# Kernel optimization log

Measured on AMD Instinct MI355X. Metric: run time of the kernel, lower is better.

The kernel has to match this reference:

```python
import jax, jax.numpy as jnp
import numpy as np

K = 7          # kernel_size
GC = 16        # group_channels (hardcoded in module)
EPS = 1e-5     # BatchNorm eps


def setup_inputs() -> dict:
    key = jax.random.key(0)
    ks = jax.random.split(key, 4)
    B, C, H, W = 4, 256, 56, 56
    Cr = C // 4                      # reduction_ratio = 4
    G = C // GC                      # groups = 16
    return {
        "x": jax.random.normal(ks[0], (B, C, H, W), jnp.float32),
        "conv1_w": jax.random.normal(ks[1], (Cr, C), jnp.float32) * 0.05,
        "bn_gamma": jnp.ones((Cr,), jnp.float32),
        "bn_beta": jnp.zeros((Cr,), jnp.float32),
        "bn_mean": jnp.zeros((Cr,), jnp.float32),
        "bn_var": jnp.ones((Cr,), jnp.float32),
        "conv2_w": jax.random.normal(ks[2], (K * K * G, Cr), jnp.float32) * 0.05,
        "conv2_b": jax.random.normal(ks[3], (K * K * G,), jnp.float32) * 0.05,
    }


def _unfold(x, k):
    # torch nn.Unfold with padding=(k-1)//2, stride=1 -> [B, C, k*k, H, W]
    B, C, H, W = x.shape
    p = (k - 1) // 2
    xp = jnp.pad(x, ((0, 0), (0, 0), (p, p), (p, p)))
    patches = jnp.stack(
        [xp[:, :, i:i + H, j:j + W] for i in range(k) for j in range(k)],
        axis=2,
    )  # (kh, kw) flattened, channel-slowest -> matches torch unfold layout
    return patches


def reference(x, conv1_w, bn_gamma, bn_beta, bn_mean, bn_var, conv2_w, conv2_b):
    B, C, H, W = x.shape
    G = C // GC
    # kernel-generation branch (stride == 1, no avgpool)
    w = jnp.einsum('bchw,oc->bohw', x, conv1_w)                 # conv1 1x1
    inv_std = jax.lax.rsqrt(bn_var + EPS)
    w = (w - bn_mean[None, :, None, None]) * (bn_gamma * inv_std)[None, :, None, None] \
        + bn_beta[None, :, None, None]                           # BN (eval)
    w = jax.nn.relu(w)
    w = jnp.einsum('bchw,oc->bohw', w, conv2_w) + conv2_b[None, :, None, None]
    w = w.reshape(B, G, K * K, H, W)                             # [B,G,K2,H,W]
    # unfold + weighted reduce
    patches = _unfold(x, K).reshape(B, G, GC, K * K, H, W)       # [B,G,gc,K2,H,W]
    out = jnp.einsum('bgkhw,bgckhw->bgchw', w, patches)          # sum over K2
    return out.reshape(B, C, H, W)
```

## Files before the change

### kernel.cpp

```cpp
#include <hip/hip_runtime.h>


#define EPS 1e-5f

typedef __fp16 half2t __attribute__((ext_vector_type(2)));
typedef __fp16 half4t __attribute__((ext_vector_type(4)));
typedef __fp16 half8t __attribute__((ext_vector_type(8)));
typedef float floatx4 __attribute__((ext_vector_type(4)));

__global__ __launch_bounds__(256) void k0_setup(
    const float* __restrict__ w1, const float* __restrict__ gamma,
    const float* __restrict__ beta, const float* __restrict__ mean,
    const float* __restrict__ var, const float* __restrict__ cw,
    __fp16* __restrict__ w1fh, float* __restrict__ b1f,
    __fp16* __restrict__ cwb)
{
    const int tid = blockIdx.x * 256 + threadIdx.x;
    const int n   = gridDim.x * 256;
    for (int idx = tid; idx < 16384; idx += n) {
        int c2 = idx >> 7, r = idx & 127, o = r >> 1, c = 2 * c2 + (r & 1);
        float s = gamma[o] * rsqrtf(var[o] + EPS);
        w1fh[idx] = (__fp16)(w1[o * 256 + c] * s);
    }
    for (int idx = tid; idx < 64; idx += n) {
        float s = gamma[idx] * rsqrtf(var[idx] + EPS);
        b1f[idx] = beta[idx] - mean[idx] * s;
    }
    for (int idx = tid; idx < 65536; idx += n) {
        int g = idx >> 12, k = (idx >> 6) & 63, c = idx & 63;
        cwb[idx] = (__fp16)((k < 49) ? cw[(g * 49 + k) * 64 + c] : 0.f);
    }
}

__global__ __launch_bounds__(256, 4) void k1_conv1(
    const float* __restrict__ x, const __fp16* __restrict__ w1fh,
    const float* __restrict__ b1f, __fp16* __restrict__ mid)
{
    __shared__ __align__(16) __fp16 lx2[32 * 136];
    __shared__ __align__(16) __fp16 lwh[32 * 128];
    const int t   = threadIdx.x;
    const int b   = blockIdx.y;
    const int p0  = blockIdx.x * 64;
    const int o4  = (t >> 4) * 4;
    const int px4 = (t & 15) * 4;
    float acc[4][4] = {};

    for (int c0 = 0; c0 < 256; c0 += 64) {
        {
            int c2 = t >> 3, px8 = (t & 7) * 8;
            const float* r0 = &x[(size_t)(b * 256 + c0 + 2 * c2) * 3136 + p0 + px8];
            const float* r1 = r0 + 3136;
            float4 a0 = *(const float4*)r0, a1 = *(const float4*)(r0 + 4);
            float4 b0 = *(const float4*)r1, b1 = *(const float4*)(r1 + 4);
            half8t lo, hi;
            half2t q;
            q = __builtin_amdgcn_cvt_pkrtz(a0.x, b0.x); lo[0]=q[0]; lo[1]=q[1];
            q = __builtin_amdgcn_cvt_pkrtz(a0.y, b0.y); lo[2]=q[0]; lo[3]=q[1];
            q = __builtin_amdgcn_cvt_pkrtz(a0.z, b0.z); lo[4]=q[0]; lo[5]=q[1];
            q = __builtin_amdgcn_cvt_pkrtz(a0.w, b0.w); lo[6]=q[0]; lo[7]=q[1];
            q = __builtin_amdgcn_cvt_pkrtz(a1.x, b1.x); hi[0]=q[0]; hi[1]=q[1];
            q = __builtin_amdgcn_cvt_pkrtz(a1.y, b1.y); hi[2]=q[0]; hi[3]=q[1];
            q = __builtin_amdgcn_cvt_pkrtz(a1.z, b1.z); hi[4]=q[0]; hi[5]=q[1];
            q = __builtin_amdgcn_cvt_pkrtz(a1.w, b1.w); hi[6]=q[0]; hi[7]=q[1];
            *(half8t*)&lx2[c2 * 136 + px8 * 2]     = lo;
            *(half8t*)&lx2[c2 * 136 + px8 * 2 + 8] = hi;
        }
#pragma unroll
        for (int i = 0; i < 2; ++i) {
            int s = t + i * 256;
            *(half8t*)&lwh[s * 8] = *(const half8t*)&w1fh[c0 * 64 + s * 8];
        }
        __syncthreads();
#pragma unroll 4
        for (int c2 = 0; c2 < 32; ++c2) {
            half8t mv = *(const half8t*)&lx2[c2 * 136 + px4 * 2];
            half8t wv = *(const half8t*)&lwh[c2 * 128 + o4 * 2];
            half2t mp[4], wp[4];
#pragma unroll
            for (int j = 0; j < 4; ++j) {
                mp[j][0] = mv[2 * j]; mp[j][1] = mv[2 * j + 1];
                wp[j][0] = wv[2 * j]; wp[j][1] = wv[2 * j + 1];
            }
#pragma unroll
            for (int i = 0; i < 4; ++i)
#pragma unroll
                for (int j = 0; j < 4; ++j)
                    acc[i][j] = __builtin_amdgcn_fdot2(wp[i], mp[j], acc[i][j], false);
        }
        __syncthreads();
    }
    float bb[4];
#pragma unroll
    for (int i = 0; i < 4; ++i) bb[i] = b1f[o4 + i];
#pragma unroll
    for (int j = 0; j < 4; ++j) {
        int p = p0 + px4 + j;
        float v0 = fmaxf(acc[0][j] + bb[0], 0.f);
        float v1 = fmaxf(acc[1][j] + bb[1], 0.f);
        float v2 = fmaxf(acc[2][j] + bb[2], 0.f);
        float v3 = fmaxf(acc[3][j] + bb[3], 0.f);
        half2t u0 = __builtin_amdgcn_cvt_pkrtz(v0, v1);
        half2t u1 = __builtin_amdgcn_cvt_pkrtz(v2, v3);
        half4t h; h[0] = u0[0]; h[1] = u0[1]; h[2] = u1[0]; h[3] = u1[1];
        *(half4t*)&mid[(size_t)(b * 3136 + p) * 64 + o4] = h;
    }
}

__global__ __launch_bounds__(256, 5) void k23_fused(
    const float* __restrict__ x, const __fp16* __restrict__ mid,
    const __fp16* __restrict__ cwb, const float* __restrict__ cb,
    float* __restrict__ out)
{
    __shared__ __align__(16) unsigned char smem[31760];
    __fp16* lmid = (__fp16*)smem;
    __fp16* lwk  = (__fp16*)(smem + 9216);
    float*  lx   = (float*)smem;
    float*  lw2  = (float*)(smem + 18432);

    const int t  = threadIdx.x;
    const int b  = blockIdx.z;
    const int g  = blockIdx.y;
    const int th = blockIdx.x / 7, tw = blockIdx.x % 7;
    const int h0 = th * 8, w0 = tw * 8;

#pragma unroll
    for (int i = 0; i < 2; ++i) {
        int s  = t + i * 256;
        int px = s >> 3, c8 = s & 7;
        int pix = (h0 + (px >> 3)) * 56 + w0 + (px & 7);
        *(half8t*)&lmid[px * 72 + c8 * 8] =
            *(const half8t*)&mid[(size_t)(b * 3136 + pix) * 64 + c8 * 8];
    }
#pragma unroll
    for (int i = 0; i < 2; ++i) {
        int s = t + i * 256;
        int k = s >> 3, c8 = s & 7;
        *(half8t*)&lwk[k * 72 + c8 * 8] = *(const half8t*)&cwb[g * 4096 + s * 8];
    }
    float rv[13];
#pragma unroll
    for (int i = 0; i < 13; ++i) {
        int idx = t + i * 256;
        float v = 0.f;
        if (idx < 3136) {
            int ch = idx / 196, r = idx % 196;
            int rr = r / 14, col = r % 14;
            int gh = h0 + rr - 3, gw = w0 + col - 3;
            if (gh >= 0 && gh < 56 && gw >= 0 && gw < 56)
                v = x[(b * 256 + g * 16 + ch) * 3136 + gh * 56 + gw];
        }
        rv[i] = v;
    }
    __syncthreads();

    {
        const int lane = t & 63, wvid = t >> 6;
        const int mrow = lane & 15, quad = lane >> 4;
        half8t a0 = *(const half8t*)&lwk[(wvid * 16 + mrow) * 72 + quad * 8];
        half8t a1 = *(const half8t*)&lwk[(wvid * 16 + mrow) * 72 + quad * 8 + 32];
        float bias[4];
        int   kor[4];
#pragma unroll
        for (int i = 0; i < 4; ++i) {
            kor[i]  = wvid * 16 + quad * 4 + i;
            bias[i] = (kor[i] < 49) ? cb[g * 49 + kor[i]] : 0.f;
        }
#pragma unroll
        for (int pt = 0; pt < 4; ++pt) {
            half8t b0 = *(const half8t*)&lmid[(pt * 16 + mrow) * 72 + quad * 8];
            half8t b1 = *(const half8t*)&lmid[(pt * 16 + mrow) * 72 + quad * 8 + 32];
            floatx4 acc = {0.f, 0.f, 0.f, 0.f};
            acc = __builtin_amdgcn_mfma_f32_16x16x32_f16(a0, b0, acc, 0, 0, 0);
            acc = __builtin_amdgcn_mfma_f32_16x16x32_f16(a1, b1, acc, 0, 0, 0);
#pragma unroll
            for (int i = 0; i < 4; ++i)
                if (kor[i] < 49)
                    lw2[kor[i] * 68 + pt * 16 + mrow] = acc[i] + bias[i];
        }
    }
    __syncthreads();

#pragma unroll
    for (int i = 0; i < 13; ++i) {
        int idx = t + i * 256;
        if (idx < 3136) {
            int ch = idx / 196, r = idx % 196;
            lx[ch * 232 + (r / 14) * 15 + (r % 14)] = rv[i];
        }
    }
    __syncthreads();

    const int cc = t >> 4, pxt = t & 15;
    const int sh = pxt >> 1, sw4 = (pxt & 1) * 4;
    float a0 = 0.f, a1 = 0.f, a2 = 0.f, a3 = 0.f;
#pragma unroll
    for (int kh = 0; kh < 7; ++kh) {
        float xr[10];
        const int base = cc * 232 + (sh + kh) * 15 + sw4;
#pragma unroll
        for (int j = 0; j < 10; ++j) xr[j] = lx[base + j];
#pragma unroll
        for (int kw = 0; kw < 7; ++kw) {
            const float4 wv = *(const float4*)&lw2[(kh * 7 + kw) * 68 + pxt * 4];
            a0 = fmaf(wv.x, xr[kw + 0], a0);
            a1 = fmaf(wv.y, xr[kw + 1], a1);
            a2 = fmaf(wv.z, xr[kw + 2], a2);
            a3 = fmaf(wv.w, xr[kw + 3], a3);
        }
    }
    *(float4*)&out[(b * 256 + g * 16 + cc) * 3136 + (h0 + sh) * 56 + w0 + sw4] =
        make_float4(a0, a1, a2, a3);
}

extern "C" void kernel_launch(void* const* d_in, const int* in_sizes, int n_in,
                              void* d_out, int out_size, void* d_ws, size_t ws_size,
                              hipStream_t stream) {
    const float* x     = (const float*)d_in[0];
    const float* w1    = (const float*)d_in[1];
    const float* gamma = (const float*)d_in[2];
    const float* beta  = (const float*)d_in[3];
    const float* mean  = (const float*)d_in[4];
    const float* var   = (const float*)d_in[5];
    const float* cw    = (const float*)d_in[6];
    const float* cb    = (const float*)d_in[7];
    float* out = (float*)d_out;

    unsigned char* ws = (unsigned char*)d_ws;
    __fp16* mid  = (__fp16*)(ws);
    __fp16* w1fh = (__fp16*)(ws + 1605632);
    float*  b1f  = (float*)(ws + 1638400);
    __fp16* cwb  = (__fp16*)(ws + 1638656);

    k0_setup<<<dim3(64), 256, 0, stream>>>(w1, gamma, beta, mean, var, cw,
                                           w1fh, b1f, cwb);
    k1_conv1<<<dim3(49, 4), 256, 0, stream>>>(x, w1fh, b1f, mid);
    k23_fused<<<dim3(49, 16, 4), 256, 0, stream>>>(x, mid, cwb, cb, out);
}
```

Baseline: 113.5 us.

## Use MFMA for conv1, load conv2 weights directly, vectorize unfold LDS reads

Rewrites the 1x1 conv1 kernel to use 16x16x32 fp16 MFMA with weights held in registers instead of fdot2 on CUDA-style tiles. The output is staged through LDS for coalesced half8 stores, and the setup kernel's weight layout changes to row-major to match. In the fused kernel, conv2 A-fragments are loaded straight from global memory instead of through LDS, which shrinks shared memory. The x tile row pitch changes to 16 so that rows can be read as float4. The risks are lower occupancy in conv1 (launch bounds drop to 2) and reduced overlap of the global weight loads.

```diff
diff --git a/kernel.cpp b/kernel.cpp
--- a/kernel.cpp
+++ b/kernel.cpp
@@ -4,7 +4,6 @@
 #define EPS 1e-5f
 
 typedef __fp16 half2t __attribute__((ext_vector_type(2)));
-typedef __fp16 half4t __attribute__((ext_vector_type(4)));
 typedef __fp16 half8t __attribute__((ext_vector_type(8)));
 typedef float floatx4 __attribute__((ext_vector_type(4)));
 
@@ -18,9 +17,9 @@
     const int tid = blockIdx.x * 256 + threadIdx.x;
     const int n   = gridDim.x * 256;
     for (int idx = tid; idx < 16384; idx += n) {
-        int c2 = idx >> 7, r = idx & 127, o = r >> 1, c = 2 * c2 + (r & 1);
+        int o = idx >> 8;
         float s = gamma[o] * rsqrtf(var[o] + EPS);
-        w1fh[idx] = (__fp16)(w1[o * 256 + c] * s);
+        w1fh[idx] = (__fp16)(w1[idx] * s);
     }
     for (int idx = tid; idx < 64; idx += n) {
         float s = gamma[idx] * rsqrtf(var[idx] + EPS);
@@ -32,77 +31,73 @@
     }
 }
 
-__global__ __launch_bounds__(256, 4) void k1_conv1(
+__global__ __launch_bounds__(256, 2) void k1_conv1(
     const float* __restrict__ x, const __fp16* __restrict__ w1fh,
     const float* __restrict__ b1f, __fp16* __restrict__ mid)
 {
-    __shared__ __align__(16) __fp16 lx2[32 * 136];
-    __shared__ __align__(16) __fp16 lwh[32 * 128];
-    const int t   = threadIdx.x;
-    const int b   = blockIdx.y;
-    const int p0  = blockIdx.x * 64;
-    const int o4  = (t >> 4) * 4;
-    const int px4 = (t & 15) * 4;
-    float acc[4][4] = {};
-
-    for (int c0 = 0; c0 < 256; c0 += 64) {
-        {
-            int c2 = t >> 3, px8 = (t & 7) * 8;
-            const float* r0 = &x[(size_t)(b * 256 + c0 + 2 * c2) * 3136 + p0 + px8];
-            const float* r1 = r0 + 3136;
-            float4 a0 = *(const float4*)r0, a1 = *(const float4*)(r0 + 4);
-            float4 b0 = *(const float4*)r1, b1 = *(const float4*)(r1 + 4);
-            half8t lo, hi;
-            half2t q;
-            q = __builtin_amdgcn_cvt_pkrtz(a0.x, b0.x); lo[0]=q[0]; lo[1]=q[1];
-            q = __builtin_amdgcn_cvt_pkrtz(a0.y, b0.y); lo[2]=q[0]; lo[3]=q[1];
-            q = __builtin_amdgcn_cvt_pkrtz(a0.z, b0.z); lo[4]=q[0]; lo[5]=q[1];
-            q = __builtin_amdgcn_cvt_pkrtz(a0.w, b0.w); lo[6]=q[0]; lo[7]=q[1];
-            q = __builtin_amdgcn_cvt_pkrtz(a1.x, b1.x); hi[0]=q[0]; hi[1]=q[1];
-            q = __builtin_amdgcn_cvt_pkrtz(a1.y, b1.y); hi[2]=q[0]; hi[3]=q[1];
-            q = __builtin_amdgcn_cvt_pkrtz(a1.z, b1.z); hi[4]=q[0]; hi[5]=q[1];
-            q = __builtin_amdgcn_cvt_pkrtz(a1.w, b1.w); hi[6]=q[0]; hi[7]=q[1];
-            *(half8t*)&lx2[c2 * 136 + px8 * 2]     = lo;
-            *(half8t*)&lx2[c2 * 136 + px8 * 2 + 8] = hi;
-        }
-#pragma unroll
-        for (int i = 0; i < 2; ++i) {
-            int s = t + i * 256;
-            *(half8t*)&lwh[s * 8] = *(const half8t*)&w1fh[c0 * 64 + s * 8];
+    __shared__ __align__(16) __fp16 lxB[64 * 72];
+    const int t    = threadIdx.x;
+    const int b    = blockIdx.y;
+    const int p0   = blockIdx.x * 64;
+    const int lane = t & 63, wvid = t >> 6;
+    const int mrow = lane & 15, quad = lane >> 4;
+
+    const int orow = wvid * 16 + mrow;
+    half8t A[4][2];
+#pragma unroll
+    for (int ch = 0; ch < 4; ++ch)
+#pragma unroll
+        for (int h = 0; h < 2; ++h)
+            A[ch][h] = *(const half8t*)&w1fh[orow * 256 + ch * 64 + h * 32 + quad * 8];
+
+    floatx4 acc[4] = {};
+    const int c2 = t & 31, pxo = t >> 5;
+    for (int ch = 0; ch < 4; ++ch) {
+        const float* r0 = &x[(size_t)(b * 256 + ch * 64 + 2 * c2) * 3136 + p0 + pxo * 8];
+        const float* r1 = r0 + 3136;
+        float4 a0 = *(const float4*)r0, a1 = *(const float4*)(r0 + 4);
+        float4 b0 = *(const float4*)r1, b1 = *(const float4*)(r1 + 4);
+        const float* f0 = (const float*)&a0;
+        const float* f1 = (const float*)&b0;
+#pragma unroll
+        for (int j = 0; j < 4; ++j) {
+            half2t q = __builtin_amdgcn_cvt_pkrtz(f0[j], f1[j]);
+            *(half2t*)&lxB[(pxo * 8 + j) * 72 + 2 * c2] = q;
+        }
+        const float* g0 = (const float*)&a1;
+        const float* g1 = (const float*)&b1;
+#pragma unroll
+        for (int j = 0; j < 4; ++j) {
+            half2t q = __builtin_amdgcn_cvt_pkrtz(g0[j], g1[j]);
+            *(half2t*)&lxB[(pxo * 8 + 4 + j) * 72 + 2 * c2] = q;
         }
         __syncthreads();
-#pragma unroll 4
-        for (int c2 = 0; c2 < 32; ++c2) {
-            half8t mv = *(const half8t*)&lx2[c2 * 136 + px4 * 2];
-            half8t wv = *(const half8t*)&lwh[c2 * 128 + o4 * 2];
-            half2t mp[4], wp[4];
-#pragma unroll
-            for (int j = 0; j < 4; ++j) {
-                mp[j][0] = mv[2 * j]; mp[j][1] = mv[2 * j + 1];
-                wp[j][0] = wv[2 * j]; wp[j][1] = wv[2 * j + 1];
-            }
-#pragma unroll
-            for (int i = 0; i < 4; ++i)
-#pragma unroll
-                for (int j = 0; j < 4; ++j)
-                    acc[i][j] = __builtin_amdgcn_fdot2(wp[i], mp[j], acc[i][j], false);
+#pragma unroll
+        for (int pt = 0; pt < 4; ++pt) {
+            half8t bf0 = *(const half8t*)&lxB[(pt * 16 + mrow) * 72 + quad * 8];
+            half8t bf1 = *(const half8t*)&lxB[(pt * 16 + mrow) * 72 + quad * 8 + 32];
+            acc[pt] = __builtin_amdgcn_mfma_f32_16x16x32_f16(A[ch][0], bf0, acc[pt], 0, 0, 0);
+            acc[pt] = __builtin_amdgcn_mfma_f32_16x16x32_f16(A[ch][1], bf1, acc[pt], 0, 0, 0);
         }
         __syncthreads();
     }
     float bb[4];
 #pragma unroll
-    for (int i = 0; i < 4; ++i) bb[i] = b1f[o4 + i];
-#pragma unroll
-    for (int j = 0; j < 4; ++j) {
-        int p = p0 + px4 + j;
-        float v0 = fmaxf(acc[0][j] + bb[0], 0.f);
-        float v1 = fmaxf(acc[1][j] + bb[1], 0.f);
-        float v2 = fmaxf(acc[2][j] + bb[2], 0.f);
-        float v3 = fmaxf(acc[3][j] + bb[3], 0.f);
-        half2t u0 = __builtin_amdgcn_cvt_pkrtz(v0, v1);
-        half2t u1 = __builtin_amdgcn_cvt_pkrtz(v2, v3);
-        half4t h; h[0] = u0[0]; h[1] = u0[1]; h[2] = u1[0]; h[3] = u1[1];
-        *(half4t*)&mid[(size_t)(b * 3136 + p) * 64 + o4] = h;
+    for (int i = 0; i < 4; ++i) bb[i] = b1f[wvid * 16 + quad * 4 + i];
+#pragma unroll
+    for (int pt = 0; pt < 4; ++pt)
+#pragma unroll
+        for (int i = 0; i < 4; ++i) {
+            float v = fmaxf(acc[pt][i] + bb[i], 0.f);
+            lxB[(pt * 16 + mrow) * 72 + wvid * 16 + quad * 4 + i] = (__fp16)v;
+        }
+    __syncthreads();
+#pragma unroll
+    for (int it = 0; it < 2; ++it) {
+        int slot = t + it * 256;
+        int px = slot >> 3, o8 = slot & 7;
+        *(half8t*)&mid[(size_t)(b * 3136 + p0 + px) * 64 + o8 * 8] =
+            *(const half8t*)&lxB[px * 72 + o8 * 8];
     }
 }
 
@@ -111,17 +106,21 @@
     const __fp16* __restrict__ cwb, const float* __restrict__ cb,
     float* __restrict__ out)
 {
-    __shared__ __align__(16) unsigned char smem[31760];
+    __shared__ __align__(16) unsigned char smem[27920];
     __fp16* lmid = (__fp16*)smem;
-    __fp16* lwk  = (__fp16*)(smem + 9216);
     float*  lx   = (float*)smem;
-    float*  lw2  = (float*)(smem + 18432);
+    float*  lw2  = (float*)(smem + 14592);
 
     const int t  = threadIdx.x;
     const int b  = blockIdx.z;
     const int g  = blockIdx.y;
     const int th = blockIdx.x / 7, tw = blockIdx.x % 7;
     const int h0 = th * 8, w0 = tw * 8;
+    const int lane = t & 63, wvid = t >> 6;
+    const int mrow = lane & 15, quad = lane >> 4;
+
+    half8t a0 = *(const half8t*)&cwb[g * 4096 + (wvid * 16 + mrow) * 64 + quad * 8];
+    half8t a1 = *(const half8t*)&cwb[g * 4096 + (wvid * 16 + mrow) * 64 + quad * 8 + 32];
 
 #pragma unroll
     for (int i = 0; i < 2; ++i) {
@@ -130,12 +129,6 @@
         int pix = (h0 + (px >> 3)) * 56 + w0 + (px & 7);
         *(half8t*)&lmid[px * 72 + c8 * 8] =
             *(const half8t*)&mid[(size_t)(b * 3136 + pix) * 64 + c8 * 8];
-    }
-#pragma unroll
-    for (int i = 0; i < 2; ++i) {
-        int s = t + i * 256;
-        int k = s >> 3, c8 = s & 7;
-        *(half8t*)&lwk[k * 72 + c8 * 8] = *(const half8t*)&cwb[g * 4096 + s * 8];
     }
     float rv[13];
 #pragma unroll
@@ -154,10 +147,6 @@
     __syncthreads();
 
     {
-        const int lane = t & 63, wvid = t >> 6;
-        const int mrow = lane & 15, quad = lane >> 4;
-        half8t a0 = *(const half8t*)&lwk[(wvid * 16 + mrow) * 72 + quad * 8];
-        half8t a1 = *(const half8t*)&lwk[(wvid * 16 + mrow) * 72 + quad * 8 + 32];
         float bias[4];
         int   kor[4];
 #pragma unroll
@@ -185,31 +174,35 @@
         int idx = t + i * 256;
         if (idx < 3136) {
             int ch = idx / 196, r = idx % 196;
-            lx[ch * 232 + (r / 14) * 15 + (r % 14)] = rv[i];
+            lx[ch * 228 + (r / 14) * 16 + (r % 14)] = rv[i];
         }
     }
     __syncthreads();
 
     const int cc = t >> 4, pxt = t & 15;
     const int sh = pxt >> 1, sw4 = (pxt & 1) * 4;
-    float a0 = 0.f, a1 = 0.f, a2 = 0.f, a3 = 0.f;
+    float a0f = 0.f, a1f = 0.f, a2f = 0.f, a3f = 0.f;
 #pragma unroll
     for (int kh = 0; kh < 7; ++kh) {
-        float xr[10];
-        const int base = cc * 232 + (sh + kh) * 15 + sw4;
-#pragma unroll
-        for (int j = 0; j < 10; ++j) xr[j] = lx[base + j];
+        const float* row = &lx[cc * 228 + (sh + kh) * 16 + sw4];
+        float4 x0 = *(const float4*)row;
+        float4 x1 = *(const float4*)(row + 4);
+        float4 x2 = *(const float4*)(row + 8);
+        float xr[12];
+        xr[0] = x0.x; xr[1] = x0.y; xr[2]  = x0.z; xr[3]  = x0.w;
+        xr[4] = x1.x; xr[5] = x1.y; xr[6]  = x1.z; xr[7]  = x1.w;
+        xr[8] = x2.x; xr[9] = x2.y; xr[10] = x2.z; xr[11] = x2.w;
 #pragma unroll
         for (int kw = 0; kw < 7; ++kw) {
             const float4 wv = *(const float4*)&lw2[(kh * 7 + kw) * 68 + pxt * 4];
-            a0 = fmaf(wv.x, xr[kw + 0], a0);
-            a1 = fmaf(wv.y, xr[kw + 1], a1);
-            a2 = fmaf(wv.z, xr[kw + 2], a2);
-            a3 = fmaf(wv.w, xr[kw + 3], a3);
+            a0f = fmaf(wv.x, xr[kw + 0], a0f);
+            a1f = fmaf(wv.y, xr[kw + 1], a1f);
+            a2f = fmaf(wv.z, xr[kw + 2], a2f);
+            a3f = fmaf(wv.w, xr[kw + 3], a3f);
         }
     }
     *(float4*)&out[(b * 256 + g * 16 + cc) * 3136 + (h0 + sh) * 56 + w0 + sw4] =
-        make_float4(a0, a1, a2, a3);
+        make_float4(a0f, a1f, a2f, a3f);
 }
 
 extern "C" void kernel_launch(void* const* d_in, const int* in_sizes, int n_in,
```

New measurement: 121.2 us. 1.07x slower.
